# Kernel tuning notes

Measured on AMD Instinct MI355X. Metric: run time of the kernel, lower is better.

The kernel has to match this reference:

```python
import jax, jax.numpy as jnp
import numpy as np

N_HEAD = 16
LN_EPS = 1e-5


def setup_inputs() -> dict:
    key = jax.random.key(0)
    ks = jax.random.split(key, 12)
    B, S, D = 4, 1024, 1024
    s = 1.0 / np.sqrt(D)
    return {
        "Q": jax.random.normal(ks[0], (B, S, D), jnp.float32),
        "K": jax.random.normal(ks[1], (B, S, D), jnp.float32),
        "V": jax.random.normal(ks[2], (B, S, D), jnp.float32),
        # Linear weights stored torch-style [out, in]
        "Wq": jax.random.normal(ks[3], (D, D), jnp.float32) * s,
        "bq": jnp.zeros((D,), jnp.float32),
        "Wk": jax.random.normal(ks[4], (D, D), jnp.float32) * s,
        "bk": jnp.zeros((D,), jnp.float32),
        "Wv": jax.random.normal(ks[5], (D, D), jnp.float32) * s,
        "bv": jnp.zeros((D,), jnp.float32),
        "Wo": jax.random.normal(ks[6], (D, D), jnp.float32) * s,
        "bo": jnp.zeros((D,), jnp.float32),
        "ln_g": jnp.ones((D,), jnp.float32),
        "ln_b": jnp.zeros((D,), jnp.float32),
    }


def _layer_norm(x, g, b):
    mu = jnp.mean(x, axis=-1, keepdims=True)
    var = jnp.mean(jnp.square(x - mu), axis=-1, keepdims=True)
    return (x - mu) * jax.lax.rsqrt(var + LN_EPS) * g + b


def reference(Q, K, V, Wq, bq, Wk, bk, Wv, bv, Wo, bo, ln_g, ln_b):
    B, S, D = Q.shape
    H = N_HEAD
    dk = D // H
    # projections, split heads: [B, H, S, dk]
    q = (Q @ Wq.T + bq).reshape(B, S, H, dk).transpose(0, 2, 1, 3)
    k = (K @ Wk.T + bk).reshape(B, S, H, dk).transpose(0, 2, 1, 3)
    v = (V @ Wv.T + bv).reshape(B, S, H, dk).transpose(0, 2, 1, 3)
    scores = jnp.einsum("bhqd,bhkd->bhqk", q, k) / np.sqrt(dk)
    # NOTE: original module applies softmax twice (F.softmax then nn.Softmax)
    attn = jax.nn.softmax(jax.nn.softmax(scores, axis=-1), axis=-1)
    ctx = jnp.einsum("bhqk,bhkd->bhqd", attn, v)  # [B, H, S, dk]
    ctx = ctx.transpose(0, 2, 1, 3).reshape(B, S, D)
    out = ctx @ Wo.T + bo
    return _layer_norm(out + Q, ln_g, ln_b)
```

## Files before the change

kernel.cpp:

```cpp
#include <hip/hip_runtime.h>
#include <cstdint>
#include <cstddef>


typedef unsigned short ushort_t;
typedef __attribute__((ext_vector_type(8))) short bf16x8;
typedef __attribute__((ext_vector_type(8))) unsigned short us8;
typedef __attribute__((ext_vector_type(4))) unsigned short us4;
typedef __attribute__((ext_vector_type(4))) float f32x4;

#define MFMA16(a, b, c) __builtin_amdgcn_mfma_f32_16x16x32_bf16((a), (b), (c), 0, 0, 0)
#define EXP2F(x) __builtin_amdgcn_exp2f(x)
#define LOG2E 1.4426950408889634f

__device__ __forceinline__ float b2f(ushort_t u) {
  union { unsigned int i; float f; } x; x.i = ((unsigned int)u) << 16; return x.f;
}
__device__ __forceinline__ ushort_t f2b(float f) {
  union { unsigned int i; float f; } x; x.f = f;
  unsigned int r = (x.i + 0x7FFFu + ((x.i >> 16) & 1u)) >> 16;
  return (ushort_t)r;
}
__device__ __forceinline__ unsigned int cvtpk(float lo, float hi) {
  unsigned int r;
  asm("v_cvt_pk_bf16_f32 %0, %1, %2" : "=v"(r) : "v"(lo), "v"(hi));
  return r;
}
__device__ __forceinline__ us8 cvt8pk(float4 a, float4 b) {
  union { unsigned int u[4]; us8 v; } r;
  r.u[0] = cvtpk(a.x, a.y); r.u[1] = cvtpk(a.z, a.w);
  r.u[2] = cvtpk(b.x, b.y); r.u[3] = cvtpk(b.z, b.w);
  return r.v;
}

__device__ __forceinline__ void gll16(const ushort_t* g, ushort_t* l) {
  __builtin_amdgcn_global_load_lds(
      (const __attribute__((address_space(1))) void*)g,
      (__attribute__((address_space(3))) void*)l, 16, 0, 0);
}

__global__ __launch_bounds__(256, 8) void cvt4_kernel(
    const float* __restrict__ w0, const float* __restrict__ w1,
    const float* __restrict__ w2, const float* __restrict__ w3,
    ushort_t* __restrict__ dst) {
  const int which = blockIdx.y;
  const float* src = (which == 0) ? w0 : (which == 1) ? w1 : (which == 2) ? w2 : w3;
  const int i = (blockIdx.x * 256 + threadIdx.x) * 8;
  const float4 a = *(const float4*)(src + i);
  const float4 b = *(const float4*)(src + i + 4);
  *(us8*)(dst + (size_t)which * 1048576 + i) = cvt8pk(a, b);
}

__global__ __launch_bounds__(256, 3) void qkv_proj_kernel(
    const float* __restrict__ Qin, const float* __restrict__ Kin,
    const float* __restrict__ Vin,
    const ushort_t* __restrict__ wq, const ushort_t* __restrict__ wk,
    const ushort_t* __restrict__ wv,
    const float* __restrict__ bq, const float* __restrict__ bk,
    const float* __restrict__ bv,
    ushort_t* __restrict__ qb, ushort_t* __restrict__ kb,
    ushort_t* __restrict__ vb) {
  __shared__ __align__(16) ushort_t Asl0[128 * 32];
  __shared__ __align__(16) ushort_t Asl1[128 * 32];
  __shared__ __align__(16) ushort_t Bsl0[128 * 32];
  __shared__ __align__(16) ushort_t Bsl1[128 * 32];
  const float* A; const ushort_t* W; const float* bias; float scale;
  if (blockIdx.z == 0)      { A = Qin; W = wq; bias = bq; scale = 0.125f * LOG2E; }
  else if (blockIdx.z == 1) { A = Kin; W = wk; bias = bk; scale = 1.0f; }
  else                      { A = Vin; W = wv; bias = bv; scale = 1.0f; }
  const int l = blockIdx.x;
  const int xcd = l & 7, ii = l >> 3;
  const int m0 = (xcd * 4 + (ii >> 3)) * 128;
  const int n0 = (ii & 7) * 128;
  const int tid = threadIdx.x;
  const int wave = tid >> 6, lane = tid & 63;
  const int l15 = lane & 15, quad = lane >> 4;
  const int wr = wave >> 1, wc = wave & 1;

  const int ra = tid >> 2, ca = (tid & 3) * 8;
  const float* Ap0 = A + (size_t)(m0 + ra) * 1024 + ca;
  const float* Ap1 = A + (size_t)(m0 + ra + 64) * 1024 + ca;

  const ushort_t* Bg0 = W + (size_t)(n0 + wave * 32 + (lane >> 2)) * 1024 + (lane & 3) * 8;
  const ushort_t* Bg1 = W + (size_t)(n0 + wave * 32 + 16 + (lane >> 2)) * 1024 + (lane & 3) * 8;

  float4 xa0 = *(const float4*)(Ap0), xa1 = *(const float4*)(Ap0 + 4);
  float4 xa2 = *(const float4*)(Ap1), xa3 = *(const float4*)(Ap1 + 4);
  gll16(Bg0, Bsl0 + wave * 1024);
  gll16(Bg1, Bsl0 + wave * 1024 + 512);
  *(us8*)(Asl0 + ra * 32 + ca) = cvt8pk(xa0, xa1);
  *(us8*)(Asl0 + (ra + 64) * 32 + ca) = cvt8pk(xa2, xa3);
  float4 ya0 = *(const float4*)(Ap0 + 32), ya1 = *(const float4*)(Ap0 + 36);
  float4 ya2 = *(const float4*)(Ap1 + 32), ya3 = *(const float4*)(Ap1 + 36);
  __syncthreads();

  f32x4 acc[4][4] = {};
#define QKV_COMPUTE(ASL, BSL)                                                   \
  {                                                                             \
    bf16x8 af[4], bfr[4];                                                       \
    _Pragma("unroll") for (int s = 0; s < 4; ++s)                               \
        af[s] = *(const bf16x8*)((ASL) + (wr * 64 + s * 16 + l15) * 32 + quad * 8); \
    _Pragma("unroll") for (int s = 0; s < 4; ++s)                               \
        bfr[s] = *(const bf16x8*)((BSL) + (wc * 64 + s * 16 + l15) * 32 + quad * 8); \
    _Pragma("unroll") for (int ms = 0; ms < 4; ++ms)                            \
        _Pragma("unroll") for (int ns = 0; ns < 4; ++ns)                        \
            acc[ms][ns] = MFMA16(af[ms], bfr[ns], acc[ms][ns]);                 \
  }

  for (int k0 = 0; k0 < 1024; k0 += 64) {
    {
      gll16(Bg0 + k0 + 32, Bsl1 + wave * 1024);
      gll16(Bg1 + k0 + 32, Bsl1 + wave * 1024 + 512);
      *(us8*)(Asl1 + ra * 32 + ca) = cvt8pk(ya0, ya1);
      *(us8*)(Asl1 + (ra + 64) * 32 + ca) = cvt8pk(ya2, ya3);
    }
    if (k0 + 64 < 1024) {
      xa0 = *(const float4*)(Ap0 + k0 + 64); xa1 = *(const float4*)(Ap0 + k0 + 68);
      xa2 = *(const float4*)(Ap1 + k0 + 64); xa3 = *(const float4*)(Ap1 + k0 + 68);
    }
    QKV_COMPUTE(Asl0, Bsl0)
    __syncthreads();
    if (k0 + 64 < 1024) {
      gll16(Bg0 + k0 + 64, Bsl0 + wave * 1024);
      gll16(Bg1 + k0 + 64, Bsl0 + wave * 1024 + 512);
      *(us8*)(Asl0 + ra * 32 + ca) = cvt8pk(xa0, xa1);
      *(us8*)(Asl0 + (ra + 64) * 32 + ca) = cvt8pk(xa2, xa3);
      if (k0 + 96 < 1024) {
        ya0 = *(const float4*)(Ap0 + k0 + 96); ya1 = *(const float4*)(Ap0 + k0 + 100);
        ya2 = *(const float4*)(Ap1 + k0 + 96); ya3 = *(const float4*)(Ap1 + k0 + 100);
      }
    }
    QKV_COMPUTE(Asl1, Bsl1)
    __syncthreads();
  }
#undef QKV_COMPUTE

  if (blockIdx.z != 2) {
    ushort_t* outp = (blockIdx.z == 0) ? qb : kb;
#pragma unroll
    for (int ns = 0; ns < 4; ++ns) {
      const int col = n0 + wc * 64 + ns * 16 + l15;
      const float bv_ = bias[col];
#pragma unroll
      for (int ms = 0; ms < 4; ++ms) {
        const int rowb = m0 + wr * 64 + ms * 16 + quad * 4;
#pragma unroll
        for (int r = 0; r < 4; ++r) {
          outp[(size_t)(rowb + r) * 1024 + col] =
              f2b((acc[ms][ns][r] + bv_) * scale);
        }
      }
    }
  } else {
#pragma unroll
    for (int ns = 0; ns < 4; ++ns) {
      const int col = n0 + wc * 64 + ns * 16 + l15;
      const float bv_ = bias[col];
      const int h = col >> 6, d = col & 63;
#pragma unroll
      for (int ms = 0; ms < 4; ++ms) {
        const int i0 = m0 + wr * 64 + ms * 16 + quad * 4;
        const int b = i0 >> 10, s0 = i0 & 1023;
        us4 pack;
#pragma unroll
        for (int r = 0; r < 4; ++r) pack[r] = f2b(acc[ms][ns][r] + bv_);
        *(us4*)(vb + ((size_t)(b * 16 + h) * 64 + d) * 1024 + s0) = pack;
      }
    }
  }
}

__global__ __launch_bounds__(256, 4) void attn_kernel(
    const ushort_t* __restrict__ qb, const ushort_t* __restrict__ kb,
    const ushort_t* __restrict__ vb, ushort_t* __restrict__ ctx) {
  __shared__ __align__(16) ushort_t Qs[64 * 72];
  __shared__ __align__(16) ushort_t Ks[64 * 72];
  __shared__ __align__(16) ushort_t Vt[64 * 72];

  const int tid = threadIdx.x, wave = tid >> 6, lane = tid & 63;
  const int l15 = lane & 15, quad = lane >> 4;
  const int l = blockIdx.x;
  const int xcd = l & 7, ii = l >> 3;
  const int bh = xcd * 8 + (ii >> 4);
  const int q0 = (ii & 15) * 64;
  const int b = bh >> 4, h = bh & 15;
  const ushort_t* qg = qb + ((size_t)b << 20) + h * 64;
  const ushort_t* kg = kb + ((size_t)b << 20) + h * 64;
  const ushort_t* vg = vb + ((size_t)bh << 16);

  const int kr0 = tid >> 3, kc0 = (tid & 7) * 8;
  const int kr1 = (tid + 256) >> 3, kc1 = kc0;

  *(us8*)(Qs + kr0 * 72 + kc0) = *(const us8*)(qg + (size_t)(q0 + kr0) * 1024 + kc0);
  *(us8*)(Qs + kr1 * 72 + kc1) = *(const us8*)(qg + (size_t)(q0 + kr1) * 1024 + kc1);
  __syncthreads();
  bf16x8 aqh[2];
  aqh[0] = *(const bf16x8*)(Qs + (wave * 16 + l15) * 72 + quad * 8);
  aqh[1] = *(const bf16x8*)(Qs + (wave * 16 + l15) * 72 + 32 + quad * 8);

  float z1 = 0.f;
  us8 rk0 = *(const us8*)(kg + (size_t)kr0 * 1024 + kc0);
  us8 rk1 = *(const us8*)(kg + (size_t)kr1 * 1024 + kc1);
  for (int kt = 0; kt < 16; ++kt) {
    __syncthreads();
    *(us8*)(Ks + kr0 * 72 + kc0) = rk0;
    *(us8*)(Ks + kr1 * 72 + kc1) = rk1;
    __syncthreads();
    if (kt < 15) {
      rk0 = *(const us8*)(kg + (size_t)((kt + 1) * 64 + kr0) * 1024 + kc0);
      rk1 = *(const us8*)(kg + (size_t)((kt + 1) * 64 + kr1) * 1024 + kc1);
    }
    f32x4 sc[4] = {};
#pragma unroll
    for (int kk = 0; kk < 2; ++kk) {
#pragma unroll
      for (int ns = 0; ns < 4; ++ns) {
        const bf16x8 kf = *(const bf16x8*)(Ks + (ns * 16 + l15) * 72 + kk * 32 + quad * 8);
        sc[ns] = MFMA16(kf, aqh[kk], sc[ns]);
      }
    }
#pragma unroll
    for (int ns = 0; ns < 4; ++ns)
#pragma unroll
      for (int r = 0; r < 4; ++r) z1 += EXP2F(sc[ns][r]);
  }
  z1 += __shfl_xor(z1, 16, 64);
  z1 += __shfl_xor(z1, 32, 64);
  const float iz1 = LOG2E / z1;

  const int adr0 = ((((quad & 1) << 1) * 16) + l15) << 2;
  const int adr1 = adr0 + 64;

  f32x4 oac[4] = {};
  float z2 = 0.f;
  rk0 = *(const us8*)(kg + (size_t)kr0 * 1024 + kc0);
  rk1 = *(const us8*)(kg + (size_t)kr1 * 1024 + kc1);
  us8 rv0 = *(const us8*)(vg + (size_t)kr0 * 1024 + kc0);
  us8 rv1 = *(const us8*)(vg + (size_t)kr1 * 1024 + kc1);
  for (int kt = 0; kt < 16; ++kt) {
    __syncthreads();
    *(us8*)(Ks + kr0 * 72 + kc0) = rk0;
    *(us8*)(Ks + kr1 * 72 + kc1) = rk1;
    *(us8*)(Vt + kr0 * 72 + kc0) = rv0;
    *(us8*)(Vt + kr1 * 72 + kc1) = rv1;
    __syncthreads();
    if (kt < 15) {
      rk0 = *(const us8*)(kg + (size_t)((kt + 1) * 64 + kr0) * 1024 + kc0);
      rk1 = *(const us8*)(kg + (size_t)((kt + 1) * 64 + kr1) * 1024 + kc1);
      rv0 = *(const us8*)(vg + (size_t)kr0 * 1024 + (kt + 1) * 64 + kc0);
      rv1 = *(const us8*)(vg + (size_t)kr1 * 1024 + (kt + 1) * 64 + kc1);
    }
    f32x4 sc[4] = {};
#pragma unroll
    for (int kk = 0; kk < 2; ++kk) {
#pragma unroll
      for (int ns = 0; ns < 4; ++ns) {
        const bf16x8 kf = *(const bf16x8*)(Ks + (ns * 16 + l15) * 72 + kk * 32 + quad * 8);
        sc[ns] = MFMA16(kf, aqh[kk], sc[ns]);
      }
    }
    unsigned int D[4][2];
#pragma unroll
    for (int ns = 0; ns < 4; ++ns) {
      const float e0 = EXP2F(EXP2F(sc[ns][0]) * iz1);
      const float e1 = EXP2F(EXP2F(sc[ns][1]) * iz1);
      const float e2 = EXP2F(EXP2F(sc[ns][2]) * iz1);
      const float e3 = EXP2F(EXP2F(sc[ns][3]) * iz1);
      z2 += (e0 + e1) + (e2 + e3);
      D[ns][0] = cvtpk(e0, e1);
      D[ns][1] = cvtpk(e2, e3);
    }
#pragma unroll
    for (int kk = 0; kk < 2; ++kk) {
      union { unsigned int u[4]; bf16x8 v; } pf;
#pragma unroll
      for (int t = 0; t < 4; ++t) {
        const int adr = (t >> 1) ? adr1 : adr0;
        const int lo = __builtin_amdgcn_ds_bpermute(adr, (int)D[2 * kk][t & 1]);
        const int hi = __builtin_amdgcn_ds_bpermute(adr, (int)D[2 * kk + 1][t & 1]);
        pf.u[t] = (unsigned int)((quad >= 2) ? hi : lo);
      }
#pragma unroll
      for (int ns2 = 0; ns2 < 4; ++ns2) {
        const bf16x8 vf = *(const bf16x8*)(Vt + (ns2 * 16 + l15) * 72 + kk * 32 + quad * 8);
        oac[ns2] = MFMA16(vf, pf.v, oac[ns2]);
      }
    }
  }

  z2 += __shfl_xor(z2, 16, 64);
  z2 += __shfl_xor(z2, 32, 64);
  const int s = q0 + wave * 16 + l15;
  ushort_t* crow = ctx + ((size_t)(b * 1024 + s)) * 1024 + h * 64;
#pragma unroll
  for (int ns2 = 0; ns2 < 4; ++ns2) {
    us4 pack;
#pragma unroll
    for (int r = 0; r < 4; ++r) pack[r] = f2b(oac[ns2][r] / z2);
    *(us4*)(crow + ns2 * 16 + quad * 4) = pack;
  }
}

__global__ __launch_bounds__(256, 4) void out_proj_kernel(
    const ushort_t* __restrict__ ctxp, const ushort_t* __restrict__ wo,
    const float* __restrict__ bo, ushort_t* __restrict__ pre) {
  __shared__ __align__(16) ushort_t Asl0[64 * 32];
  __shared__ __align__(16) ushort_t Asl1[64 * 32];
  __shared__ __align__(16) ushort_t Bsl0[128 * 32];
  __shared__ __align__(16) ushort_t Bsl1[128 * 32];
  const int tid = threadIdx.x;
  const int wave = tid >> 6, lane = tid & 63;
  const int l15 = lane & 15, quad = lane >> 4;
  const int wr = wave >> 1, wc = wave & 1;
  const int l = blockIdx.x;
  const int xcd = l & 7, ii = l >> 3;
  const int m0 = (xcd * 8 + (ii >> 3)) * 64;
  const int n0 = (ii & 7) * 128;

  const ushort_t* Ag = ctxp + (size_t)(m0 + wave * 16 + (lane >> 2)) * 1024 + (lane & 3) * 8;
  const ushort_t* Bg0 = wo + (size_t)(n0 + wave * 32 + (lane >> 2)) * 1024 + (lane & 3) * 8;
  const ushort_t* Bg1 = wo + (size_t)(n0 + wave * 32 + 16 + (lane >> 2)) * 1024 + (lane & 3) * 8;

  gll16(Ag, Asl0 + wave * 512);
  gll16(Bg0, Bsl0 + wave * 1024);
  gll16(Bg1, Bsl0 + wave * 1024 + 512);
  __syncthreads();

  f32x4 acc[2][4] = {};
#define OUTP_COMPUTE(ASL, BSL)                                                  \
  {                                                                             \
    bf16x8 af[2], bfr[4];                                                       \
    _Pragma("unroll") for (int s = 0; s < 2; ++s)                               \
        af[s] = *(const bf16x8*)((ASL) + (wr * 32 + s * 16 + l15) * 32 + quad * 8); \
    _Pragma("unroll") for (int s = 0; s < 4; ++s)                               \
        bfr[s] = *(const bf16x8*)((BSL) + (wc * 64 + s * 16 + l15) * 32 + quad * 8); \
    _Pragma("unroll") for (int ms = 0; ms < 2; ++ms)                            \
        _Pragma("unroll") for (int ns = 0; ns < 4; ++ns)                        \
            acc[ms][ns] = MFMA16(af[ms], bfr[ns], acc[ms][ns]);                 \
  }

  for (int k0 = 0; k0 < 1024; k0 += 64) {
    {
      gll16(Ag + k0 + 32, Asl1 + wave * 512);
      gll16(Bg0 + k0 + 32, Bsl1 + wave * 1024);
      gll16(Bg1 + k0 + 32, Bsl1 + wave * 1024 + 512);
    }
    OUTP_COMPUTE(Asl0, Bsl0)
    __syncthreads();
    if (k0 + 64 < 1024) {
      gll16(Ag + k0 + 64, Asl0 + wave * 512);
      gll16(Bg0 + k0 + 64, Bsl0 + wave * 1024);
      gll16(Bg1 + k0 + 64, Bsl0 + wave * 1024 + 512);
    }
    OUTP_COMPUTE(Asl1, Bsl1)
    __syncthreads();
  }
#undef OUTP_COMPUTE

#pragma unroll
  for (int ns = 0; ns < 4; ++ns) {
    const int col = n0 + wc * 64 + ns * 16 + l15;
    const float bv_ = bo[col];
#pragma unroll
    for (int ms = 0; ms < 2; ++ms) {
      const int rowb = m0 + wr * 32 + ms * 16 + quad * 4;
#pragma unroll
      for (int r = 0; r < 4; ++r) {
        pre[(size_t)(rowb + r) * 1024 + col] = f2b(acc[ms][ns][r] + bv_);
      }
    }
  }
}

__global__ __launch_bounds__(256, 4) void ln_kernel(
    const ushort_t* __restrict__ pre, const float* __restrict__ Q,
    const float* __restrict__ g, const float* __restrict__ bta,
    float* __restrict__ out) {
  const int row = blockIdx.x;
  const int tid = threadIdx.x;
  const size_t base = (size_t)row * 1024 + tid * 4;
  const ushort4 p4 = *(const ushort4*)(pre + base);
  const float4 q4 = *(const float4*)(Q + base);
  float v[4] = {b2f(p4.x) + q4.x, b2f(p4.y) + q4.y,
                b2f(p4.z) + q4.z, b2f(p4.w) + q4.w};
  float s1 = v[0] + v[1] + v[2] + v[3];
  float s2 = v[0]*v[0] + v[1]*v[1] + v[2]*v[2] + v[3]*v[3];
#pragma unroll
  for (int off = 1; off < 64; off <<= 1) {
    s1 += __shfl_xor(s1, off, 64);
    s2 += __shfl_xor(s2, off, 64);
  }
  __shared__ float r1[4], r2[4];
  const int wave = tid >> 6, lane = tid & 63;
  if (lane == 0) { r1[wave] = s1; r2[wave] = s2; }
  __syncthreads();
  const float t1 = r1[0] + r1[1] + r1[2] + r1[3];
  const float t2 = r2[0] + r2[1] + r2[2] + r2[3];
  const float mu = t1 * (1.0f / 1024.0f);
  const float var = t2 * (1.0f / 1024.0f) - mu * mu;
  const float inv = rsqrtf(var + 1e-5f);
  const int c0 = tid * 4;
#pragma unroll
  for (int j = 0; j < 4; ++j) {
    const int c = c0 + j;
    out[(size_t)row * 1024 + c] = (v[j] - mu) * inv * g[c] + bta[c];
  }
}

extern "C" void kernel_launch(void* const* d_in, const int* in_sizes, int n_in,
                              void* d_out, int out_size, void* d_ws, size_t ws_size,
                              hipStream_t stream) {
  const float* Q  = (const float*)d_in[0];
  const float* K  = (const float*)d_in[1];
  const float* V  = (const float*)d_in[2];
  const float* Wq = (const float*)d_in[3];
  const float* bq = (const float*)d_in[4];
  const float* Wk = (const float*)d_in[5];
  const float* bk = (const float*)d_in[6];
  const float* Wv = (const float*)d_in[7];
  const float* bv = (const float*)d_in[8];
  const float* Wo = (const float*)d_in[9];
  const float* bo = (const float*)d_in[10];
  const float* lg = (const float*)d_in[11];
  const float* lb = (const float*)d_in[12];

  char* ws = (char*)d_ws;
  ushort_t* qb  = (ushort_t*)(ws);
  ushort_t* kb  = (ushort_t*)(ws + ((size_t)8  << 20));
  ushort_t* vb  = (ushort_t*)(ws + ((size_t)16 << 20));
  ushort_t* pre = (ushort_t*)(ws);

  ushort_t* dptr  = (ushort_t*)d_out;
  ushort_t* wo_bf = dptr;
  ushort_t* wq_bf = dptr + 1048576;
  ushort_t* wk_bf = dptr + 2097152;
  ushort_t* wv_bf = dptr + 3145728;
  ushort_t* ctx   = dptr + 4194304;
  float*    out   = (float*)d_out;

  cvt4_kernel<<<dim3(512, 4), 256, 0, stream>>>(Wo, Wq, Wk, Wv, dptr);
  qkv_proj_kernel<<<dim3(256, 1, 3), 256, 0, stream>>>(Q, K, V, wq_bf, wk_bf, wv_bf,
                                                       bq, bk, bv, qb, kb, vb);
  attn_kernel<<<dim3(1024), 256, 0, stream>>>(qb, kb, vb, ctx);
  out_proj_kernel<<<dim3(512), 256, 0, stream>>>(ctx, wo_bf, bo, pre);
  ln_kernel<<<dim3(4096), 256, 0, stream>>>(pre, Q, lg, lb, out);
}
```

Baseline: 236.9 us.

## Double-buffer K/V tiles in attention and relax QKV GEMM barrier waits

The attention kernel now holds two shared-memory buffers each for K and V. The next tile is stored to LDS while the current one is used, which removes one of the two barriers per iteration, and global loads are prefetched two tiles ahead. The QKV projection kernel swaps __syncthreads for an explicit s_waitcnt with a partial vmcnt plus s_barrier, so in-flight global prefetches need not drain at each barrier. This raises LDS use in the attention kernel from three tiles to four, which may affect occupancy, and hand-written waitcnt counts could be wrong if the compiler reorders memory operations.

```diff
diff --git a/kernel.cpp b/kernel.cpp
--- a/kernel.cpp
+++ b/kernel.cpp
@@ -92,7 +92,8 @@
   *(us8*)(Asl0 + (ra + 64) * 32 + ca) = cvt8pk(xa2, xa3);
   float4 ya0 = *(const float4*)(Ap0 + 32), ya1 = *(const float4*)(Ap0 + 36);
   float4 ya2 = *(const float4*)(Ap1 + 32), ya3 = *(const float4*)(Ap1 + 36);
-  __syncthreads();
+  asm volatile("s_waitcnt vmcnt(4) lgkmcnt(0)" ::: "memory");
+  __builtin_amdgcn_s_barrier();
 
   f32x4 acc[4][4] = {};
 #define QKV_COMPUTE(ASL, BSL)                                                   \
@@ -119,7 +120,9 @@
       xa2 = *(const float4*)(Ap1 + k0 + 64); xa3 = *(const float4*)(Ap1 + k0 + 68);
     }
     QKV_COMPUTE(Asl0, Bsl0)
-    __syncthreads();
+    if (k0 + 64 < 1024) asm volatile("s_waitcnt vmcnt(4) lgkmcnt(0)" ::: "memory");
+    else                asm volatile("s_waitcnt vmcnt(0) lgkmcnt(0)" ::: "memory");
+    __builtin_amdgcn_s_barrier();
     if (k0 + 64 < 1024) {
       gll16(Bg0 + k0 + 64, Bsl0 + wave * 1024);
       gll16(Bg1 + k0 + 64, Bsl0 + wave * 1024 + 512);
@@ -131,7 +134,9 @@
       }
     }
     QKV_COMPUTE(Asl1, Bsl1)
-    __syncthreads();
+    if (k0 + 96 < 1024)      asm volatile("s_waitcnt vmcnt(4) lgkmcnt(0)" ::: "memory");
+    else                     asm volatile("s_waitcnt vmcnt(0) lgkmcnt(0)" ::: "memory");
+    __builtin_amdgcn_s_barrier();
   }
 #undef QKV_COMPUTE
 
@@ -173,9 +178,10 @@
 __global__ __launch_bounds__(256, 4) void attn_kernel(
     const ushort_t* __restrict__ qb, const ushort_t* __restrict__ kb,
     const ushort_t* __restrict__ vb, ushort_t* __restrict__ ctx) {
-  __shared__ __align__(16) ushort_t Qs[64 * 72];
-  __shared__ __align__(16) ushort_t Ks[64 * 72];
-  __shared__ __align__(16) ushort_t Vt[64 * 72];
+  __shared__ __align__(16) ushort_t Sh0[64 * 72];
+  __shared__ __align__(16) ushort_t Sh1[64 * 72];
+  __shared__ __align__(16) ushort_t Sh2[64 * 72];
+  __shared__ __align__(16) ushort_t Sh3[64 * 72];
 
   const int tid = threadIdx.x, wave = tid >> 6, lane = tid & 63;
   const int l15 = lane & 15, quad = lane >> 4;
@@ -190,39 +196,48 @@
 
   const int kr0 = tid >> 3, kc0 = (tid & 7) * 8;
   const int kr1 = (tid + 256) >> 3, kc1 = kc0;
-
-  *(us8*)(Qs + kr0 * 72 + kc0) = *(const us8*)(qg + (size_t)(q0 + kr0) * 1024 + kc0);
-  *(us8*)(Qs + kr1 * 72 + kc1) = *(const us8*)(qg + (size_t)(q0 + kr1) * 1024 + kc1);
+  const int o0 = kr0 * 72 + kc0, o1 = kr1 * 72 + kc1;
+
+  *(us8*)(Sh0 + o0) = *(const us8*)(qg + (size_t)(q0 + kr0) * 1024 + kc0);
+  *(us8*)(Sh0 + o1) = *(const us8*)(qg + (size_t)(q0 + kr1) * 1024 + kc1);
+  us8 rk0 = *(const us8*)(kg + (size_t)kr0 * 1024 + kc0);
+  us8 rk1 = *(const us8*)(kg + (size_t)kr1 * 1024 + kc1);
+  *(us8*)(Sh1 + o0) = rk0;
+  *(us8*)(Sh1 + o1) = rk1;
+  rk0 = *(const us8*)(kg + (size_t)(64 + kr0) * 1024 + kc0);
+  rk1 = *(const us8*)(kg + (size_t)(64 + kr1) * 1024 + kc1);
   __syncthreads();
   bf16x8 aqh[2];
-  aqh[0] = *(const bf16x8*)(Qs + (wave * 16 + l15) * 72 + quad * 8);
-  aqh[1] = *(const bf16x8*)(Qs + (wave * 16 + l15) * 72 + 32 + quad * 8);
+  aqh[0] = *(const bf16x8*)(Sh0 + (wave * 16 + l15) * 72 + quad * 8);
+  aqh[1] = *(const bf16x8*)(Sh0 + (wave * 16 + l15) * 72 + 32 + quad * 8);
 
   float z1 = 0.f;
-  us8 rk0 = *(const us8*)(kg + (size_t)kr0 * 1024 + kc0);
-  us8 rk1 = *(const us8*)(kg + (size_t)kr1 * 1024 + kc1);
   for (int kt = 0; kt < 16; ++kt) {
-    __syncthreads();
-    *(us8*)(Ks + kr0 * 72 + kc0) = rk0;
-    *(us8*)(Ks + kr1 * 72 + kc1) = rk1;
-    __syncthreads();
+    const ushort_t* kcur = (kt & 1) ? Sh2 : Sh1;
+    f32x4 sc[4] = {};
+#pragma unroll
+    for (int kk = 0; kk < 2; ++kk) {
+#pragma unroll
+      for (int ns = 0; ns < 4; ++ns) {
+        const bf16x8 kf = *(const bf16x8*)(kcur + (ns * 16 + l15) * 72 + kk * 32 + quad * 8);
+        sc[ns] = MFMA16(kf, aqh[kk], sc[ns]);
+      }
+    }
     if (kt < 15) {
-      rk0 = *(const us8*)(kg + (size_t)((kt + 1) * 64 + kr0) * 1024 + kc0);
-      rk1 = *(const us8*)(kg + (size_t)((kt + 1) * 64 + kr1) * 1024 + kc1);
-    }
-    f32x4 sc[4] = {};
-#pragma unroll
-    for (int kk = 0; kk < 2; ++kk) {
-#pragma unroll
-      for (int ns = 0; ns < 4; ++ns) {
-        const bf16x8 kf = *(const bf16x8*)(Ks + (ns * 16 + l15) * 72 + kk * 32 + quad * 8);
-        sc[ns] = MFMA16(kf, aqh[kk], sc[ns]);
+      ushort_t* knxt = (kt & 1) ? Sh1 : Sh2;
+      *(us8*)(knxt + o0) = rk0;
+      *(us8*)(knxt + o1) = rk1;
+      if (kt < 14) {
+        rk0 = *(const us8*)(kg + (size_t)((kt + 2) * 64 + kr0) * 1024 + kc0);
+        rk1 = *(const us8*)(kg + (size_t)((kt + 2) * 64 + kr1) * 1024 + kc1);
       }
     }
 #pragma unroll
     for (int ns = 0; ns < 4; ++ns)
 #pragma unroll
       for (int r = 0; r < 4; ++r) z1 += EXP2F(sc[ns][r]);
+    asm volatile("s_waitcnt lgkmcnt(0)" ::: "memory");
+    __builtin_amdgcn_s_barrier();
   }
   z1 += __shfl_xor(z1, 16, 64);
   z1 += __shfl_xor(z1, 32, 64);
@@ -237,26 +252,41 @@
   rk1 = *(const us8*)(kg + (size_t)kr1 * 1024 + kc1);
   us8 rv0 = *(const us8*)(vg + (size_t)kr0 * 1024 + kc0);
   us8 rv1 = *(const us8*)(vg + (size_t)kr1 * 1024 + kc1);
+  *(us8*)(Sh0 + o0) = rk0;
+  *(us8*)(Sh0 + o1) = rk1;
+  *(us8*)(Sh2 + o0) = rv0;
+  *(us8*)(Sh2 + o1) = rv1;
+  rk0 = *(const us8*)(kg + (size_t)(64 + kr0) * 1024 + kc0);
+  rk1 = *(const us8*)(kg + (size_t)(64 + kr1) * 1024 + kc1);
+  rv0 = *(const us8*)(vg + (size_t)kr0 * 1024 + 64 + kc0);
+  rv1 = *(const us8*)(vg + (size_t)kr1 * 1024 + 64 + kc1);
+  asm volatile("s_waitcnt lgkmcnt(0)" ::: "memory");
+  __builtin_amdgcn_s_barrier();
+
   for (int kt = 0; kt < 16; ++kt) {
-    __syncthreads();
-    *(us8*)(Ks + kr0 * 72 + kc0) = rk0;
-    *(us8*)(Ks + kr1 * 72 + kc1) = rk1;
-    *(us8*)(Vt + kr0 * 72 + kc0) = rv0;
-    *(us8*)(Vt + kr1 * 72 + kc1) = rv1;
-    __syncthreads();
+    const ushort_t* kcur = (kt & 1) ? Sh1 : Sh0;
+    const ushort_t* vcur = (kt & 1) ? Sh3 : Sh2;
+    f32x4 sc[4] = {};
+#pragma unroll
+    for (int kk = 0; kk < 2; ++kk) {
+#pragma unroll
+      for (int ns = 0; ns < 4; ++ns) {
+        const bf16x8 kf = *(const bf16x8*)(kcur + (ns * 16 + l15) * 72 + kk * 32 + quad * 8);
+        sc[ns] = MFMA16(kf, aqh[kk], sc[ns]);
+      }
+    }
     if (kt < 15) {
-      rk0 = *(const us8*)(kg + (size_t)((kt + 1) * 64 + kr0) * 1024 + kc0);
-      rk1 = *(const us8*)(kg + (size_t)((kt + 1) * 64 + kr1) * 1024 + kc1);
-      rv0 = *(const us8*)(vg + (size_t)kr0 * 1024 + (kt + 1) * 64 + kc0);
-      rv1 = *(const us8*)(vg + (size_t)kr1 * 1024 + (kt + 1) * 64 + kc1);
-    }
-    f32x4 sc[4] = {};
-#pragma unroll
-    for (int kk = 0; kk < 2; ++kk) {
-#pragma unroll
-      for (int ns = 0; ns < 4; ++ns) {
-        const bf16x8 kf = *(const bf16x8*)(Ks + (ns * 16 + l15) * 72 + kk * 32 + quad * 8);
-        sc[ns] = MFMA16(kf, aqh[kk], sc[ns]);
+      ushort_t* knxt = (kt & 1) ? Sh0 : Sh1;
+      ushort_t* vnxt = (kt & 1) ? Sh2 : Sh3;
+      *(us8*)(knxt + o0) = rk0;
+      *(us8*)(knxt + o1) = rk1;
+      *(us8*)(vnxt + o0) = rv0;
+      *(us8*)(vnxt + o1) = rv1;
+      if (kt < 14) {
+        rk0 = *(const us8*)(kg + (size_t)((kt + 2) * 64 + kr0) * 1024 + kc0);
+        rk1 = *(const us8*)(kg + (size_t)((kt + 2) * 64 + kr1) * 1024 + kc1);
+        rv0 = *(const us8*)(vg + (size_t)kr0 * 1024 + (kt + 2) * 64 + kc0);
+        rv1 = *(const us8*)(vg + (size_t)kr1 * 1024 + (kt + 2) * 64 + kc1);
       }
     }
     unsigned int D[4][2];
@@ -282,10 +312,12 @@
       }
 #pragma unroll
       for (int ns2 = 0; ns2 < 4; ++ns2) {
-        const bf16x8 vf = *(const bf16x8*)(Vt + (ns2 * 16 + l15) * 72 + kk * 32 + quad * 8);
+        const bf16x8 vf = *(const bf16x8*)(vcur + (ns2 * 16 + l15) * 72 + kk * 32 + quad * 8);
         oac[ns2] = MFMA16(vf, pf.v, oac[ns2]);
       }
     }
+    asm volatile("s_waitcnt lgkmcnt(0)" ::: "memory");
+    __builtin_amdgcn_s_barrier();
   }
 
   z2 += __shfl_xor(z2, 16, 64);
```

Result: no change. 235.4 us (-0.6%).
